# Optimization experiments

Hardware: AMD Instinct MI355X
Metric: run time of the kernel (lower is better)

The kernel has to match this reference:

```python
import math
import jax, jax.numpy as jnp
import numpy as np

N_HEAD = 16


def setup_inputs() -> dict:
    key = jax.random.key(0)
    ks = jax.random.split(key, 6)
    B, T, C = 4, 2048, 1024
    hs = C // N_HEAD
    block_size = 2048
    x = jax.random.normal(ks[0], (B, T, C), dtype=jnp.float32)
    c_attn_w = jax.random.normal(ks[1], (C, 3 * C), dtype=jnp.float32) * 0.02
    c_attn_b = jnp.zeros((3 * C,), dtype=jnp.float32)
    c_proj_w = jax.random.normal(ks[2], (C, C), dtype=jnp.float32) * (0.02 * (2 * 24) ** -0.5)
    c_proj_b = jnp.zeros((C,), dtype=jnp.float32)
    wpe = jax.random.normal(ks[3], (block_size, hs), dtype=jnp.float32) * 0.02
    return {"x": x, "c_attn_w": c_attn_w, "c_attn_b": c_attn_b,
            "c_proj_w": c_proj_w, "c_proj_b": c_proj_b, "wpe": wpe}


def reference(x, c_attn_w, c_attn_b, c_proj_w, c_proj_b, wpe):
    B, T, C = x.shape
    hs = C // N_HEAD
    # fused QKV projection
    qkv = x @ c_attn_w + c_attn_b            # [B, T, 3C]
    q, k, v = jnp.split(qkv, 3, axis=-1)
    pos_emb = wpe[:T]                        # [T, hs]
    # NOTE: faithful to original — raw reshape (not transpose) before the add
    q = (q.reshape(B, N_HEAD, T, hs) + pos_emb).reshape(B, T, N_HEAD, hs)
    k = (k.reshape(B, N_HEAD, T, hs) + pos_emb).reshape(B, T, N_HEAD, hs)
    v = v.reshape(B, T, N_HEAD, hs)
    # vanilla causal attention
    qt = jnp.transpose(q, (0, 2, 1, 3))      # [B, H, T, hs]
    kt = jnp.transpose(k, (0, 2, 3, 1))      # [B, H, hs, T]
    vt = jnp.transpose(v, (0, 2, 1, 3))      # [B, H, T, hs]
    att = qt @ kt / math.sqrt(hs)            # [B, H, T, T]
    causal = jnp.tril(jnp.ones((T, T), dtype=bool))
    att = jnp.where(causal, att, float('-inf'))
    att = jax.nn.softmax(att, axis=-1)
    y = att @ vt                             # [B, H, T, hs]
    y = jnp.transpose(y, (0, 2, 1, 3)).reshape(B, T, C)
    return y @ c_proj_w + c_proj_b
```

## Files before the change

kernel.cpp:

```cpp
#include <hip/hip_runtime.h>

typedef __attribute__((ext_vector_type(8))) short s16x8;
typedef __attribute__((ext_vector_type(4))) float f32x4;
typedef __attribute__((ext_vector_type(4))) unsigned short u16x4;

#define AS1 __attribute__((address_space(1)))
#define AS3 __attribute__((address_space(3)))

__device__ __forceinline__ unsigned short f2bf(float f) {
    union { float f; unsigned u; } c; c.f = f;
    return (unsigned short)((c.u + 0x7FFFu + ((c.u >> 16) & 1u)) >> 16);
}

__global__ void k_f32_to_bf16(const float* __restrict__ src,
                              unsigned short* __restrict__ dst, int n8) {
    int idx = blockIdx.x * 256 + threadIdx.x;
    int stride = gridDim.x * 256;
    for (int i = idx; i < n8; i += stride) {
        const float4* s = (const float4*)src + (size_t)i * 2;
        float4 a = s[0], b = s[1];
        s16x8 o;
        o[0] = (short)f2bf(a.x); o[1] = (short)f2bf(a.y);
        o[2] = (short)f2bf(a.z); o[3] = (short)f2bf(a.w);
        o[4] = (short)f2bf(b.x); o[5] = (short)f2bf(b.y);
        o[6] = (short)f2bf(b.z); o[7] = (short)f2bf(b.w);
        *((s16x8*)dst + i) = o;
    }
}

__global__ __launch_bounds__(256) void k_transpose_bf16(
    const float* __restrict__ W, unsigned short* __restrict__ Wt, int K, int N) {
    __shared__ float t[64][65];
    const int nk = K >> 6;
    const int k0 = (blockIdx.x % nk) << 6;
    const int n0 = (blockIdx.x / nk) << 6;
    const int tid = threadIdx.x;
#pragma unroll
    for (int it = 0; it < 4; it++) {
        int idx = tid + (it << 8);
        int r = idx >> 4, c4 = (idx & 15) << 2;
        float4 v = *(const float4*)(W + (size_t)(k0 + r) * N + n0 + c4);
        t[r][c4] = v.x; t[r][c4 + 1] = v.y; t[r][c4 + 2] = v.z; t[r][c4 + 3] = v.w;
    }
    __syncthreads();
#pragma unroll
    for (int it = 0; it < 2; it++) {
        int idx = tid + (it << 8);
        int rn = idx >> 3, c8 = (idx & 7) << 3;
        s16x8 o;
#pragma unroll
        for (int j = 0; j < 8; j++) o[j] = (short)f2bf(t[c8 + j][rn]);
        *(s16x8*)(Wt + (size_t)(n0 + rn) * K + k0 + c8) = o;
    }
}

__global__ __launch_bounds__(256, 2) void k_gemm_bt(
    const unsigned short* __restrict__ A, const unsigned short* __restrict__ Bt,
    const float* __restrict__ bias, const float* __restrict__ wpe,
    unsigned short* __restrict__ Qo, unsigned short* __restrict__ Ko,
    unsigned short* __restrict__ Vo, float* __restrict__ Fo,
    int N, int K, int mode) {
    __shared__ unsigned short Alds[8192];
    __shared__ unsigned short Blds[8192];
    const int tid = threadIdx.x;
    const int lane = tid & 63, wid = tid >> 6;
    const int ntile = N >> 7;
    const int chunk = (int)gridDim.x >> 3;
    const int l = ((int)blockIdx.x & 7) * chunk + ((int)blockIdx.x >> 3);
    const int m0 = (l / ntile) << 7;
    const int n0 = (l % ntile) << 7;
    const int wm = wid & 1, wn = wid >> 1;
    const int lr = lane >> 3, ls = lane & 7;
    const int l15 = lane & 15, lg = lane >> 4;

    const f32x4 vzero = {0.f, 0.f, 0.f, 0.f};
    f32x4 acc[4][4];
#pragma unroll
    for (int i = 0; i < 4; i++)
#pragma unroll
        for (int j = 0; j < 4; j++) acc[i][j] = vzero;

    for (int k0 = 0; k0 < K; k0 += 64) {
#pragma unroll
        for (int i = 0; i < 4; i++) {
            int r = (wid << 5) + (i << 3) + lr;
            int sl = (ls ^ (r & 7)) << 3;
            __builtin_amdgcn_global_load_lds(
                (const AS1 void*)(A + (size_t)(m0 + r) * K + k0 + sl),
                (AS3 void*)(Alds + (wid << 11) + (i << 9)), 16, 0, 0);
            __builtin_amdgcn_global_load_lds(
                (const AS1 void*)(Bt + (size_t)(n0 + r) * K + k0 + sl),
                (AS3 void*)(Blds + (wid << 11) + (i << 9)), 16, 0, 0);
        }
        __syncthreads();
#pragma unroll
        for (int kk = 0; kk < 2; kk++) {
            s16x8 af[4], bfr[4];
#pragma unroll
            for (int mi = 0; mi < 4; mi++) {
                int row = (wm << 6) + (mi << 4) + l15;
                int slot = lg + (kk << 2);
                af[mi] = *(const s16x8*)((const char*)Alds + row * 128 +
                                         ((slot ^ (row & 7)) << 4));
            }
#pragma unroll
            for (int ni = 0; ni < 4; ni++) {
                int row = (wn << 6) + (ni << 4) + l15;
                int slot = lg + (kk << 2);
                bfr[ni] = *(const s16x8*)((const char*)Blds + row * 128 +
                                          ((slot ^ (row & 7)) << 4));
            }
#pragma unroll
            for (int mi = 0; mi < 4; mi++)
#pragma unroll
                for (int ni = 0; ni < 4; ni++)
                    acc[mi][ni] = __builtin_amdgcn_mfma_f32_16x16x32_bf16(
                        af[mi], bfr[ni], acc[mi][ni], 0, 0, 0);
        }
        __syncthreads();
    }

    if (mode == 0) {
#pragma unroll
        for (int ni = 0; ni < 4; ni++) {
            int n = n0 + (wn << 6) + (ni << 4) + l15;
            int which = n >> 10, rem = n & 1023;
            int h = rem >> 6, s = rem & 63;
            unsigned short* out = (which == 0) ? Qo : ((which == 1) ? Ko : Vo);
            float bv = bias[n];
#pragma unroll
            for (int mi = 0; mi < 4; mi++) {
#pragma unroll
                for (int j = 0; j < 4; j++) {
                    int m = m0 + (wm << 6) + (mi << 4) + (lg << 2) + j;
                    int b = m >> 11, t = m & 2047;
                    float v = acc[mi][ni][j] + bv;
                    if (which < 2) v += wpe[((((t << 4) + h) & 2047) << 6) + s];
                    out[(size_t)(b * 16 + h) * 131072 + (size_t)t * 64 + s] = f2bf(v);
                }
            }
        }
    } else {
#pragma unroll
        for (int ni = 0; ni < 4; ni++) {
            int n = n0 + (wn << 6) + (ni << 4) + l15;
            float bv = bias[n];
#pragma unroll
            for (int mi = 0; mi < 4; mi++) {
#pragma unroll
                for (int j = 0; j < 4; j++) {
                    int m = m0 + (wm << 6) + (mi << 4) + (lg << 2) + j;
                    Fo[(size_t)m * N + n] = acc[mi][ni][j] + bv;
                }
            }
        }
    }
}

__global__ __launch_bounds__(256, 6) void k_attn(
    const unsigned short* __restrict__ Qg, const unsigned short* __restrict__ Kg,
    const unsigned short* __restrict__ Vg, unsigned short* __restrict__ Yg) {
    __shared__ unsigned short Klds[4096];
    __shared__ unsigned short Vtlds[4096];
    __shared__ unsigned short Plds[4096];
    const int tid = threadIdx.x, lane = tid & 63, wid = tid >> 6;
    const int l15 = lane & 15, lg = lane >> 4;
    const int lr = lane >> 3, ls = lane & 7;
    const int p = blockIdx.x;
    const int xcd = p & 7, rank = p >> 3;
    const int qt = 31 - (rank >> 3);
    const int bh = ((rank & 7) << 3) | xcd;
    const int b = bh >> 4, h = bh & 15;
    const size_t base = (size_t)bh * 131072;
    const int q0 = qt << 6;
    const int qrow = q0 + (wid << 4) + l15;
    const int vkv4 = (tid >> 4) << 2;
    const int vd4 = (tid & 15) << 2;

    const f32x4 vzero = {0.f, 0.f, 0.f, 0.f};

    s16x8 qf[2];
#pragma unroll
    for (int kk = 0; kk < 2; kk++)
        qf[kk] = *(const s16x8*)(Qg + base + (size_t)qrow * 64 +
                                 (kk << 5) + (lg << 3));

    f32x4 o[4];
#pragma unroll
    for (int i = 0; i < 4; i++) o[i] = vzero;
    float mrun = -3.0e38f, lrun = 0.f;

    const int nt = qt + 1;
    for (int tI = 0; tI < nt; tI++) {
        const int kv0 = tI << 6;
#pragma unroll
        for (int i = 0; i < 2; i++) {
            int r = (wid << 4) + (i << 3) + lr;
            int sl = (ls ^ (r & 7)) << 3;
            __builtin_amdgcn_global_load_lds(
                (const AS1 void*)(Kg + base + (size_t)(kv0 + r) * 64 + sl),
                (AS3 void*)(Klds + (wid << 10) + (i << 9)), 16, 0, 0);
        }
        {
            u16x4 vv[4];
#pragma unroll
            for (int r = 0; r < 4; r++)
                vv[r] = *(const u16x4*)(Vg + base +
                                        (size_t)(kv0 + vkv4 + r) * 64 + vd4);
#pragma unroll
            for (int dj = 0; dj < 4; dj++) {
                int row = vd4 + dj;
                int fv = (row ^ (row >> 3)) & 7;
                unsigned long long pk =
                    (unsigned long long)vv[0][dj] |
                    ((unsigned long long)vv[1][dj] << 16) |
                    ((unsigned long long)vv[2][dj] << 32) |
                    ((unsigned long long)vv[3][dj] << 48);
                *(unsigned long long*)((char*)Vtlds + row * 128 +
                                       ((((vkv4 >> 3) ^ fv) & 7) << 4) +
                                       ((vkv4 & 7) << 1)) = pk;
            }
        }
        __syncthreads();

        f32x4 sacc[4];
#pragma unroll
        for (int i = 0; i < 4; i++) sacc[i] = vzero;
        __builtin_amdgcn_s_setprio(1);
#pragma unroll
        for (int kk = 0; kk < 2; kk++) {
            s16x8 kf[4];
#pragma unroll
            for (int ki = 0; ki < 4; ki++) {
                int row = (ki << 4) + l15;
                int slot = lg + (kk << 2);
                kf[ki] = *(const s16x8*)((const char*)Klds + row * 128 +
                                         ((slot ^ (row & 7)) << 4));
            }
#pragma unroll
            for (int ki = 0; ki < 4; ki++)
                sacc[ki] = __builtin_amdgcn_mfma_f32_16x16x32_bf16(
                    kf[ki], qf[kk], sacc[ki], 0, 0, 0);
        }
        __builtin_amdgcn_s_setprio(0);

        float tm = -3.0e38f;
        if (tI == nt - 1) {
#pragma unroll
            for (int ki = 0; ki < 4; ki++) {
#pragma unroll
                for (int j = 0; j < 4; j++) {
                    int kvg = kv0 + (ki << 4) + (lg << 2) + j;
                    float sv = sacc[ki][j];
                    if (kvg > qrow) sv = -3.0e38f;
                    sacc[ki][j] = sv;
                    tm = fmaxf(tm, sv);
                }
            }
        } else {
#pragma unroll
            for (int ki = 0; ki < 4; ki++) {
#pragma unroll
                for (int j = 0; j < 4; j++) tm = fmaxf(tm, sacc[ki][j]);
            }
        }
        tm = fmaxf(tm, __shfl_xor(tm, 16, 64));
        tm = fmaxf(tm, __shfl_xor(tm, 32, 64));
        float mnew = fmaxf(mrun, tm);
        float rfac = __expf((mrun - mnew) * 0.125f);
        float m8 = mnew * 0.125f;
        mrun = mnew;
        float ps = 0.f;
#pragma unroll
        for (int ki = 0; ki < 4; ki++) {
#pragma unroll
            for (int j = 0; j < 4; j++) {
                float pv = __expf(__builtin_fmaf(sacc[ki][j], 0.125f, -m8));
                sacc[ki][j] = pv;
                ps += pv;
            }
        }
        ps += __shfl_xor(ps, 16, 64);
        ps += __shfl_xor(ps, 32, 64);
        lrun = lrun * rfac + ps;
#pragma unroll
        for (int j = 0; j < 4; j++) {
            float rj = __shfl(rfac, (lane & 48) | ((lg << 2) + j), 64);
#pragma unroll
            for (int si = 0; si < 4; si++) o[si][j] *= rj;
        }
#pragma unroll
        for (int ki = 0; ki < 4; ki++) {
            unsigned long long pk =
                (unsigned long long)f2bf(sacc[ki][0]) |
                ((unsigned long long)f2bf(sacc[ki][1]) << 16) |
                ((unsigned long long)f2bf(sacc[ki][2]) << 32) |
                ((unsigned long long)f2bf(sacc[ki][3]) << 48);
            int kvl = (ki << 4) + (lg << 2);
            int slot = kvl >> 3;
            *(unsigned long long*)((char*)Plds + (wid << 11) + l15 * 128 +
                                   ((slot ^ (l15 & 7)) << 4) +
                                   ((kvl & 7) << 1)) = pk;
        }

        __builtin_amdgcn_s_setprio(1);
#pragma unroll
        for (int kk = 0; kk < 2; kk++) {
            s16x8 vf[4];
#pragma unroll
            for (int si = 0; si < 4; si++) {
                int row = (si << 4) + l15;
                int slot = lg + (kk << 2);
                int fv = (row ^ (row >> 3)) & 7;
                vf[si] = *(const s16x8*)((const char*)Vtlds + row * 128 +
                                         (((slot ^ fv) & 7) << 4));
            }
            int prow = l15;
            int slot = lg + (kk << 2);
            s16x8 pf = *(const s16x8*)((const char*)Plds + (wid << 11) +
                                       prow * 128 + ((slot ^ (prow & 7)) << 4));
#pragma unroll
            for (int si = 0; si < 4; si++)
                o[si] = __builtin_amdgcn_mfma_f32_16x16x32_bf16(
                    pf, vf[si], o[si], 0, 0, 0);
        }
        __builtin_amdgcn_s_setprio(0);
        __syncthreads();
    }

#pragma unroll
    for (int j = 0; j < 4; j++) {
        float lv = __shfl(lrun, (lane & 48) | ((lg << 2) + j), 64);
        float linv = 1.0f / lv;
        int qg = q0 + (wid << 4) + (lg << 2) + j;
        size_t rowoff = ((size_t)b * 2048 + qg) * 1024 + (h << 6);
#pragma unroll
        for (int si = 0; si < 4; si++) {
            int sg = (si << 4) + l15;
            Yg[rowoff + sg] = f2bf(o[si][j] * linv);
        }
    }
}

extern "C" void kernel_launch(void* const* d_in, const int* in_sizes, int n_in,
                              void* d_out, int out_size, void* d_ws, size_t ws_size,
                              hipStream_t stream) {
    const float* x   = (const float*)d_in[0];
    const float* w1  = (const float*)d_in[1];
    const float* b1  = (const float*)d_in[2];
    const float* w2  = (const float*)d_in[3];
    const float* b2  = (const float*)d_in[4];
    const float* wpe = (const float*)d_in[5];
    float* out = (float*)d_out;

    char* ws = (char*)d_ws;
    unsigned short* xb  = (unsigned short*)(ws);
    unsigned short* w1t = (unsigned short*)(ws + 16777216);
    unsigned short* w2t = (unsigned short*)(ws + 23068672);
    unsigned short* Qb  = (unsigned short*)(ws + 25165824);
    unsigned short* Kb  = (unsigned short*)(ws + 41943040);
    unsigned short* Vb  = (unsigned short*)(ws + 58720256);
    unsigned short* Yb  = (unsigned short*)(ws + 75497472);

    k_f32_to_bf16<<<2048, 256, 0, stream>>>(x, xb, 8388608 / 8);
    k_transpose_bf16<<<768, 256, 0, stream>>>(w1, w1t, 1024, 3072);
    k_transpose_bf16<<<256, 256, 0, stream>>>(w2, w2t, 1024, 1024);
    k_gemm_bt<<<64 * 24, 256, 0, stream>>>(xb, w1t, b1, wpe, Qb, Kb, Vb,
                                           nullptr, 3072, 1024, 0);
    k_attn<<<2048, 256, 0, stream>>>(Qb, Kb, Vb, Yb);
    k_gemm_bt<<<64 * 8, 256, 0, stream>>>(Yb, w2t, b2, nullptr, nullptr, nullptr,
                                          nullptr, out, 1024, 1024, 1);
}
```

Baseline: 302.6 us.

## Rewrite projection GEMMs with 256x128 tiles and a three-stage LDS ring

```diff
diff --git a/kernel.cpp b/kernel.cpp
--- a/kernel.cpp
+++ b/kernel.cpp
@@ -54,102 +54,155 @@
     }
 }
 
-__global__ __launch_bounds__(256, 2) void k_gemm_bt(
+__global__ __launch_bounds__(512, 2) void k_gemm_ring(
     const unsigned short* __restrict__ A, const unsigned short* __restrict__ Bt,
     const float* __restrict__ bias, const float* __restrict__ wpe,
     unsigned short* __restrict__ Qo, unsigned short* __restrict__ Ko,
     unsigned short* __restrict__ Vo, float* __restrict__ Fo,
     int N, int K, int mode) {
-    __shared__ unsigned short Alds[8192];
-    __shared__ unsigned short Blds[8192];
+    __shared__ __align__(16) char smem[147456];
     const int tid = threadIdx.x;
     const int lane = tid & 63, wid = tid >> 6;
+    const int wm = wid >> 2, wn = wid & 3;
+    const int l15 = lane & 15, lg = lane >> 4;
     const int ntile = N >> 7;
     const int chunk = (int)gridDim.x >> 3;
     const int l = ((int)blockIdx.x & 7) * chunk + ((int)blockIdx.x >> 3);
-    const int m0 = (l / ntile) << 7;
+    const int m0 = (l / ntile) << 8;
     const int n0 = (l % ntile) << 7;
-    const int wm = wid & 1, wn = wid >> 1;
-    const int lr = lane >> 3, ls = lane & 7;
-    const int l15 = lane & 15, lg = lane >> 4;
+
+    const int trow = tid >> 3, tcol = tid & 7;
+    const unsigned short* pA[4];
+    const unsigned short* pB[2];
+#pragma unroll
+    for (int i = 0; i < 4; i++) {
+        int r = (i << 6) + trow;
+        pA[i] = A + (size_t)(m0 + r) * K + ((tcol ^ (r & 7)) << 3);
+    }
+#pragma unroll
+    for (int i = 0; i < 2; i++) {
+        int r = (i << 6) + trow;
+        pB[i] = Bt + (size_t)(n0 + r) * K + ((tcol ^ (r & 7)) << 3);
+    }
+    const int dA = tid << 4;
+
+    int aoff[8][2], boff[2][2];
+#pragma unroll
+    for (int mi = 0; mi < 8; mi++) {
+        int r = (wm << 7) + (mi << 4) + l15;
+#pragma unroll
+        for (int kk = 0; kk < 2; kk++)
+            aoff[mi][kk] = r * 128 + (((lg + (kk << 2)) ^ (r & 7)) << 4);
+    }
+#pragma unroll
+    for (int ni = 0; ni < 2; ni++) {
+        int r = (wn << 5) + (ni << 4) + l15;
+#pragma unroll
+        for (int kk = 0; kk < 2; kk++)
+            boff[ni][kk] = r * 128 + (((lg + (kk << 2)) ^ (r & 7)) << 4);
+    }
 
     const f32x4 vzero = {0.f, 0.f, 0.f, 0.f};
-    f32x4 acc[4][4];
-#pragma unroll
-    for (int i = 0; i < 4; i++)
-#pragma unroll
-        for (int j = 0; j < 4; j++) acc[i][j] = vzero;
-
-    for (int k0 = 0; k0 < K; k0 += 64) {
+    f32x4 acc[8][2];
+#pragma unroll
+    for (int i = 0; i < 8; i++) {
+        acc[i][0] = vzero; acc[i][1] = vzero;
+    }
+
+    auto stage = [&](int slot) {
+        char* ab = smem + slot * 32768;
+        char* bb = smem + 98304 + slot * 16384;
 #pragma unroll
         for (int i = 0; i < 4; i++) {
-            int r = (wid << 5) + (i << 3) + lr;
-            int sl = (ls ^ (r & 7)) << 3;
-            __builtin_amdgcn_global_load_lds(
-                (const AS1 void*)(A + (size_t)(m0 + r) * K + k0 + sl),
-                (AS3 void*)(Alds + (wid << 11) + (i << 9)), 16, 0, 0);
-            __builtin_amdgcn_global_load_lds(
-                (const AS1 void*)(Bt + (size_t)(n0 + r) * K + k0 + sl),
-                (AS3 void*)(Blds + (wid << 11) + (i << 9)), 16, 0, 0);
-        }
-        __syncthreads();
-#pragma unroll
-        for (int kk = 0; kk < 2; kk++) {
-            s16x8 af[4], bfr[4];
-#pragma unroll
-            for (int mi = 0; mi < 4; mi++) {
-                int row = (wm << 6) + (mi << 4) + l15;
-                int slot = lg + (kk << 2);
-                af[mi] = *(const s16x8*)((const char*)Alds + row * 128 +
-                                         ((slot ^ (row & 7)) << 4));
-            }
-#pragma unroll
-            for (int ni = 0; ni < 4; ni++) {
-                int row = (wn << 6) + (ni << 4) + l15;
-                int slot = lg + (kk << 2);
-                bfr[ni] = *(const s16x8*)((const char*)Blds + row * 128 +
-                                          ((slot ^ (row & 7)) << 4));
-            }
-#pragma unroll
-            for (int mi = 0; mi < 4; mi++)
-#pragma unroll
-                for (int ni = 0; ni < 4; ni++)
-                    acc[mi][ni] = __builtin_amdgcn_mfma_f32_16x16x32_bf16(
-                        af[mi], bfr[ni], acc[mi][ni], 0, 0, 0);
-        }
-        __syncthreads();
+            __builtin_amdgcn_global_load_lds((const AS1 void*)pA[i],
+                                             (AS3 void*)(ab + (i << 13) + dA),
+                                             16, 0, 0);
+            pA[i] += 64;
+        }
+#pragma unroll
+        for (int i = 0; i < 2; i++) {
+            __builtin_amdgcn_global_load_lds((const AS1 void*)pB[i],
+                                             (AS3 void*)(bb + (i << 13) + dA),
+                                             16, 0, 0);
+            pB[i] += 64;
+        }
+    };
+
+    const int NT = K >> 6;
+    stage(0);
+    stage(1);
+
+    for (int c = 0; c < NT; c++) {
+        if (c < NT - 1)
+            asm volatile("s_waitcnt vmcnt(6)\ns_barrier" ::: "memory");
+        else
+            asm volatile("s_waitcnt vmcnt(0)\ns_barrier" ::: "memory");
+        const int cs = c % 3;
+        const char* ab = smem + cs * 32768;
+        const char* bb = smem + 98304 + cs * 16384;
+
+        s16x8 af[8], bfr[2];
+#pragma unroll
+        for (int mi = 0; mi < 8; mi++)
+            af[mi] = *(const s16x8*)(ab + aoff[mi][0]);
+#pragma unroll
+        for (int ni = 0; ni < 2; ni++)
+            bfr[ni] = *(const s16x8*)(bb + boff[ni][0]);
+        if (c + 2 < NT) stage((c + 2) % 3);
+        __builtin_amdgcn_s_setprio(1);
+#pragma unroll
+        for (int mi = 0; mi < 8; mi++)
+#pragma unroll
+            for (int ni = 0; ni < 2; ni++)
+                acc[mi][ni] = __builtin_amdgcn_mfma_f32_16x16x32_bf16(
+                    af[mi], bfr[ni], acc[mi][ni], 0, 0, 0);
+        __builtin_amdgcn_s_setprio(0);
+#pragma unroll
+        for (int mi = 0; mi < 8; mi++)
+            af[mi] = *(const s16x8*)(ab + aoff[mi][1]);
+#pragma unroll
+        for (int ni = 0; ni < 2; ni++)
+            bfr[ni] = *(const s16x8*)(bb + boff[ni][1]);
+        __builtin_amdgcn_s_setprio(1);
+#pragma unroll
+        for (int mi = 0; mi < 8; mi++)
+#pragma unroll
+            for (int ni = 0; ni < 2; ni++)
+                acc[mi][ni] = __builtin_amdgcn_mfma_f32_16x16x32_bf16(
+                    af[mi], bfr[ni], acc[mi][ni], 0, 0, 0);
+        __builtin_amdgcn_s_setprio(0);
     }
 
     if (mode == 0) {
 #pragma unroll
-        for (int ni = 0; ni < 4; ni++) {
-            int n = n0 + (wn << 6) + (ni << 4) + l15;
+        for (int ni = 0; ni < 2; ni++) {
+            int n = n0 + (wn << 5) + (ni << 4) + l15;
             int which = n >> 10, rem = n & 1023;
             int h = rem >> 6, s = rem & 63;
-            unsigned short* out = (which == 0) ? Qo : ((which == 1) ? Ko : Vo);
+            unsigned short* outp = (which == 0) ? Qo : ((which == 1) ? Ko : Vo);
             float bv = bias[n];
 #pragma unroll
-            for (int mi = 0; mi < 4; mi++) {
+            for (int mi = 0; mi < 8; mi++) {
 #pragma unroll
                 for (int j = 0; j < 4; j++) {
-                    int m = m0 + (wm << 6) + (mi << 4) + (lg << 2) + j;
+                    int m = m0 + (wm << 7) + (mi << 4) + (lg << 2) + j;
                     int b = m >> 11, t = m & 2047;
                     float v = acc[mi][ni][j] + bv;
                     if (which < 2) v += wpe[((((t << 4) + h) & 2047) << 6) + s];
-                    out[(size_t)(b * 16 + h) * 131072 + (size_t)t * 64 + s] = f2bf(v);
+                    outp[(size_t)(b * 16 + h) * 131072 + (size_t)t * 64 + s] = f2bf(v);
                 }
             }
         }
     } else {
 #pragma unroll
-        for (int ni = 0; ni < 4; ni++) {
-            int n = n0 + (wn << 6) + (ni << 4) + l15;
+        for (int ni = 0; ni < 2; ni++) {
+            int n = n0 + (wn << 5) + (ni << 4) + l15;
             float bv = bias[n];
 #pragma unroll
-            for (int mi = 0; mi < 4; mi++) {
+            for (int mi = 0; mi < 8; mi++) {
 #pragma unroll
                 for (int j = 0; j < 4; j++) {
-                    int m = m0 + (wm << 6) + (mi << 4) + (lg << 2) + j;
+                    int m = m0 + (wm << 7) + (mi << 4) + (lg << 2) + j;
                     Fo[(size_t)m * N + n] = acc[mi][ni][j] + bv;
                 }
             }
@@ -365,9 +418,9 @@
     k_f32_to_bf16<<<2048, 256, 0, stream>>>(x, xb, 8388608 / 8);
     k_transpose_bf16<<<768, 256, 0, stream>>>(w1, w1t, 1024, 3072);
     k_transpose_bf16<<<256, 256, 0, stream>>>(w2, w2t, 1024, 1024);
-    k_gemm_bt<<<64 * 24, 256, 0, stream>>>(xb, w1t, b1, wpe, Qb, Kb, Vb,
-                                           nullptr, 3072, 1024, 0);
+    k_gemm_ring<<<768, 512, 0, stream>>>(xb, w1t, b1, wpe, Qb, Kb, Vb,
+                                         nullptr, 3072, 1024, 0);
     k_attn<<<2048, 256, 0, stream>>>(Qb, Kb, Vb, Yb);
-    k_gemm_bt<<<64 * 8, 256, 0, stream>>>(Yb, w2t, b2, nullptr, nullptr, nullptr,
-                                          nullptr, out, 1024, 1024, 1);
-}
+    k_gemm_ring<<<256, 512, 0, stream>>>(Yb, w2t, b2, nullptr, nullptr, nullptr,
+                                         nullptr, out, 1024, 1024, 1);
+}
```

New measurement: 304.6 us. Within noise of the previous version (+0.7%).
